# Optimization experiments

Hardware: AMD Instinct MI355X
Metric: run time of the kernel (lower is better)

Reference implementation:

```python
import jax, jax.numpy as jnp
import numpy as np

MASK_RATIO = 0.02
N2V_W, WAV_W, TV_W = 1.0, 0.2, 0.01
THRESHOLD = 50.0
LEVELS = 3


def setup_inputs() -> dict:
    key = jax.random.key(0)
    k1, k2, k3 = jax.random.split(key, 3)
    shape = (64, 1, 512, 512)
    pred = jax.random.uniform(k1, shape, dtype=jnp.float32)
    noisy_input = jax.random.uniform(k2, shape, dtype=jnp.float32)
    # N2V random blind-spot mask (torch.rand_like(pred) < mask_ratio)
    mask = jax.random.uniform(k3, shape, dtype=jnp.float32) < MASK_RATIO
    return {"pred": pred, "noisy_input": noisy_input, "mask": mask}


def haar_dwt2(x):
    # x: [B, H, W] with H, W even. Single-level 2D Haar DWT (pywt 'haar').
    a = x[:, 0::2, 0::2]
    b = x[:, 0::2, 1::2]
    c = x[:, 1::2, 0::2]
    d = x[:, 1::2, 1::2]
    ll = (a + b + c + d) * 0.5
    ch = (a + b - c - d) * 0.5  # horizontal detail
    cv = (a - b + c - d) * 0.5  # vertical detail
    cd = (a - b - c + d) * 0.5  # diagonal detail
    return ll, ch, cv, cd


def _level_l1(c, thr):
    # L1 between coeff and its (detached) soft-thresholded version
    target = jax.lax.stop_gradient(jnp.sign(c) * jnp.maximum(jnp.abs(c) - thr, 0.0))
    return jnp.mean(jnp.abs(c - target))


def reference(pred, noisy_input, mask):
    p = jnp.clip(pred, 0.0, 1.0)

    # --- Noise2Void masked L1 ---
    m = mask.astype(p.dtype)
    n2v = jnp.sum(jnp.abs(p - noisy_input) * m) / jnp.maximum(jnp.sum(m), 1.0)

    # --- Wavelet sparsity (multi-level Haar, soft-threshold targets) ---
    x = p[:, 0]  # [B, H, W]
    details = []  # finest first
    for _ in range(LEVELS):
        x, ch, cv, cd = haar_dwt2(x)
        details.append((ch, cv, cd))
    wav = jnp.asarray(0.0, dtype=p.dtype)
    for level_idx in range(1, LEVELS + 1):  # level_idx=1 -> coarsest (wavedec2 order)
        ch, cv, cd = details[LEVELS - level_idx]
        thr = (THRESHOLD / (2.0 ** (level_idx - 1))) / 255.0
        lvl = (_level_l1(ch, thr) + _level_l1(cv, thr) + _level_l1(cd, thr)) / 3.0
        wav = wav + (1.0 / level_idx) * lvl

    # --- Total variation ---
    tv = jnp.mean(jnp.abs(p[:, :, 1:, :] - p[:, :, :-1, :])) + \
         jnp.mean(jnp.abs(p[:, :, :, 1:] - p[:, :, :, :-1]))

    return N2V_W * n2v + WAV_W * wav + TV_W * tv
```

## Files before the change

### kernel.cpp

```cpp
#include <hip/hip_runtime.h>

#define NIMG 64
#define H 512
#define W 512

constexpr float THR_64  = 50.0f / 255.0f;
constexpr float THR_128 = 50.0f / 2.0f / 255.0f;
constexpr float THR_256 = 50.0f / 4.0f / 255.0f;

constexpr float SC_W1 = 0.2f  / 37748736.0f;
constexpr float SC_W2 = 0.2f  / 6291456.0f;
constexpr float SC_W3 = 0.2f  / 786432.0f;
constexpr float SC_TV = 0.01f / 16744448.0f;

__device__ __forceinline__ float wave_sum(float v) {
#pragma unroll
    for (int o = 32; o > 0; o >>= 1) v += __shfl_down(v, o, 64);
    return v;
}

__device__ __forceinline__ float clip01(float x) {
    return fminf(fmaxf(x, 0.0f), 1.0f);
}

__device__ __forceinline__ float4 clip4(float4 p) {
    p.x = clip01(p.x); p.y = clip01(p.y); p.z = clip01(p.z); p.w = clip01(p.w);
    return p;
}

__global__ __launch_bounds__(256) void kA(const float* __restrict__ pred,
                                          const float* __restrict__ noisy,
                                          const int* __restrict__ mask,
                                          float4* __restrict__ pA) {
    __shared__ float sl[9 * 512];
    __shared__ float sll2[2][128];
    __shared__ float red[4][3];

    const int tid = threadIdx.x;
    const int lane = tid & 63;
    const int wv = tid >> 6;
    const int bid = blockIdx.x;
    const int n = bid >> 6;
    const int s = bid & 63;
    const int r0 = s << 3;
    const size_t base = (size_t)n * (H * W) + (size_t)r0 * W;
    const size_t o0 = base + (size_t)tid * 4;

    float4 p0 = *reinterpret_cast<const float4*>(pred + o0);
    float4 p1 = *reinterpret_cast<const float4*>(pred + o0 + 1024);
    float4 p2 = *reinterpret_cast<const float4*>(pred + o0 + 2048);
    float4 p3 = *reinterpret_cast<const float4*>(pred + o0 + 3072);
    int4 m0 = *reinterpret_cast<const int4*>(mask + o0);
    int4 m1 = *reinterpret_cast<const int4*>(mask + o0 + 1024);
    int4 m2 = *reinterpret_cast<const int4*>(mask + o0 + 2048);
    int4 m3 = *reinterpret_cast<const int4*>(mask + o0 + 3072);
    if (tid < 128) {
        float4 hp = make_float4(0.f, 0.f, 0.f, 0.f);
        if (r0 > 0) {
            hp = clip4(*reinterpret_cast<const float4*>(pred + base - W + (size_t)tid * 4));
        }
        *reinterpret_cast<float4*>(&sl[(8 << 9) + (tid << 2)]) = hp;
    }

    const bool b0 = (m0.x | m0.y | m0.z | m0.w) != 0;
    const bool b1 = (m1.x | m1.y | m1.z | m1.w) != 0;
    const bool b2 = (m2.x | m2.y | m2.z | m2.w) != 0;
    const bool b3 = (m3.x | m3.y | m3.z | m3.w) != 0;
    float4 nz0 = make_float4(0.f, 0.f, 0.f, 0.f);
    float4 nz1 = nz0, nz2 = nz0, nz3 = nz0;
    if (b0) nz0 = *reinterpret_cast<const float4*>(noisy + o0);
    if (b1) nz1 = *reinterpret_cast<const float4*>(noisy + o0 + 1024);
    if (b2) nz2 = *reinterpret_cast<const float4*>(noisy + o0 + 2048);
    if (b3) nz3 = *reinterpret_cast<const float4*>(noisy + o0 + 3072);

    p0 = clip4(p0); p1 = clip4(p1); p2 = clip4(p2); p3 = clip4(p3);

    float n2v = 0.0f, msum = 0.0f;
#define ACC(P, MK, NZ)                                                           \
    {                                                                            \
        float m;                                                                 \
        m = MK.x ? 1.f : 0.f; n2v += fabsf(P.x - NZ.x) * m; msum += m;           \
        m = MK.y ? 1.f : 0.f; n2v += fabsf(P.y - NZ.y) * m; msum += m;           \
        m = MK.z ? 1.f : 0.f; n2v += fabsf(P.z - NZ.z) * m; msum += m;           \
        m = MK.w ? 1.f : 0.f; n2v += fabsf(P.w - NZ.w) * m; msum += m;           \
    }
    ACC(p0, m0, nz0)
    ACC(p1, m1, nz1)
    ACC(p2, m2, nz2)
    ACC(p3, m3, nz3)
#undef ACC
    *reinterpret_cast<float4*>(&sl[tid << 2]) = p0;
    *reinterpret_cast<float4*>(&sl[(tid + 256) << 2]) = p1;
    *reinterpret_cast<float4*>(&sl[(tid + 512) << 2]) = p2;
    *reinterpret_cast<float4*>(&sl[(tid + 768) << 2]) = p3;
    __syncthreads();

    const int q2 = wv >> 1;
    const int h = wv & 1;
    const int cofs = (h << 8) + (lane << 2);
    const float* rowp = sl + (q2 << 11);

    float4 q0 = *reinterpret_cast<const float4*>(rowp + cofs);
    float4 q1 = *reinterpret_cast<const float4*>(rowp + 512 + cofs);
    float4 qq2 = *reinterpret_cast<const float4*>(rowp + 1024 + cofs);
    float4 q3 = *reinterpret_cast<const float4*>(rowp + 1536 + cofs);
    const float* hrow = (q2 == 1) ? (sl + 3 * 512) : (sl + 8 * 512);
    float4 hl = *reinterpret_cast<const float4*>(hrow + cofs);
    const bool has_halo = (q2 == 1) || (r0 > 0);

    float tv = 0.0f;
    tv += fabsf(q0.y - q0.x) + fabsf(q0.z - q0.y) + fabsf(q0.w - q0.z);
    tv += fabsf(q1.y - q1.x) + fabsf(q1.z - q1.y) + fabsf(q1.w - q1.z);
    tv += fabsf(qq2.y - qq2.x) + fabsf(qq2.z - qq2.y) + fabsf(qq2.w - qq2.z);
    tv += fabsf(q3.y - q3.x) + fabsf(q3.z - q3.y) + fabsf(q3.w - q3.z);
    float nx0 = __shfl_down(q0.x, 1, 64);
    float nx1 = __shfl_down(q1.x, 1, 64);
    float nx2 = __shfl_down(qq2.x, 1, 64);
    float nx3 = __shfl_down(q3.x, 1, 64);
    if (lane < 63) {
        tv += fabsf(nx0 - q0.w) + fabsf(nx1 - q1.w)
            + fabsf(nx2 - qq2.w) + fabsf(nx3 - q3.w);
    } else if (h == 0) {
        tv += fabsf(rowp[256] - q0.w) + fabsf(rowp[512 + 256] - q1.w)
            + fabsf(rowp[1024 + 256] - qq2.w) + fabsf(rowp[1536 + 256] - q3.w);
    }
    tv += fabsf(q1.x - q0.x) + fabsf(q1.y - q0.y) + fabsf(q1.z - q0.z) + fabsf(q1.w - q0.w);
    tv += fabsf(qq2.x - q1.x) + fabsf(qq2.y - q1.y) + fabsf(qq2.z - q1.z) + fabsf(qq2.w - q1.w);
    tv += fabsf(q3.x - qq2.x) + fabsf(q3.y - qq2.y) + fabsf(q3.z - qq2.z) + fabsf(q3.w - qq2.w);
    if (has_halo) {
        tv += fabsf(q0.x - hl.x) + fabsf(q0.y - hl.y)
            + fabsf(q0.z - hl.z) + fabsf(q0.w - hl.w);
    }

    float wav1 = 0.0f;
    float a, b, c, d, ch, cv, cd;
    a = q0.x; b = q0.y; c = q1.x; d = q1.y;
    float llA0 = (a + b + c + d) * 0.5f;
    ch = (a + b - c - d) * 0.5f; cv = (a - b + c - d) * 0.5f; cd = (a - b - c + d) * 0.5f;
    wav1 += fminf(fabsf(ch), THR_256) + fminf(fabsf(cv), THR_256) + fminf(fabsf(cd), THR_256);
    a = q0.z; b = q0.w; c = q1.z; d = q1.w;
    float llA1 = (a + b + c + d) * 0.5f;
    ch = (a + b - c - d) * 0.5f; cv = (a - b + c - d) * 0.5f; cd = (a - b - c + d) * 0.5f;
    wav1 += fminf(fabsf(ch), THR_256) + fminf(fabsf(cv), THR_256) + fminf(fabsf(cd), THR_256);
    a = qq2.x; b = qq2.y; c = q3.x; d = q3.y;
    float llB0 = (a + b + c + d) * 0.5f;
    ch = (a + b - c - d) * 0.5f; cv = (a - b + c - d) * 0.5f; cd = (a - b - c + d) * 0.5f;
    wav1 += fminf(fabsf(ch), THR_256) + fminf(fabsf(cv), THR_256) + fminf(fabsf(cd), THR_256);
    a = qq2.z; b = qq2.w; c = q3.z; d = q3.w;
    float llB1 = (a + b + c + d) * 0.5f;
    ch = (a + b - c - d) * 0.5f; cv = (a - b + c - d) * 0.5f; cd = (a - b - c + d) * 0.5f;
    wav1 += fminf(fabsf(ch), THR_256) + fminf(fabsf(cv), THR_256) + fminf(fabsf(cd), THR_256);

    float wav2, ll2v;
    {
        a = llA0; b = llA1; c = llB0; d = llB1;
        ll2v = (a + b + c + d) * 0.5f;
        ch = (a + b - c - d) * 0.5f;
        cv = (a - b + c - d) * 0.5f;
        cd = (a - b - c + d) * 0.5f;
        wav2 = fminf(fabsf(ch), THR_128) + fminf(fabsf(cv), THR_128) + fminf(fabsf(cd), THR_128);
    }
    sll2[q2][(h << 6) + lane] = ll2v;

    float comb = wav1 * SC_W1 + wav2 * SC_W2 + tv * SC_TV;
    __syncthreads();

    if (wv == 0) {
        float2 top = *reinterpret_cast<const float2*>(&sll2[0][lane << 1]);
        float2 bot = *reinterpret_cast<const float2*>(&sll2[1][lane << 1]);
        a = top.x; b = top.y; c = bot.x; d = bot.y;
        ch = (a + b - c - d) * 0.5f;
        cv = (a - b + c - d) * 0.5f;
        cd = (a - b - c + d) * 0.5f;
        comb += (fminf(fabsf(ch), THR_64) + fminf(fabsf(cv), THR_64)
               + fminf(fabsf(cd), THR_64)) * SC_W3;
    }

    float v0 = wave_sum(n2v);
    float v1 = wave_sum(msum);
    float v2 = wave_sum(comb);
    if (lane == 0) {
        red[wv][0] = v0; red[wv][1] = v1; red[wv][2] = v2;
    }
    __syncthreads();
    if (tid == 0) {
        pA[bid] = make_float4(red[0][0] + red[1][0] + red[2][0] + red[3][0],
                              red[0][1] + red[1][1] + red[2][1] + red[3][1],
                              red[0][2] + red[1][2] + red[2][2] + red[3][2],
                              0.0f);
    }
}

__global__ __launch_bounds__(256) void kD(const float4* __restrict__ pA,
                                          float* __restrict__ out) {
    __shared__ float red[4][3];
    const int tid = threadIdx.x;
    const int lane = tid & 63, wv = tid >> 6;

    float s0 = 0, s1 = 0, s2 = 0;
#pragma unroll
    for (int j = 0; j < 16; ++j) {
        float4 v = pA[tid + (j << 8)];
        s0 += v.x; s1 += v.y; s2 += v.z;
    }
    s0 = wave_sum(s0); s1 = wave_sum(s1); s2 = wave_sum(s2);
    if (lane == 0) {
        red[wv][0] = s0; red[wv][1] = s1; red[wv][2] = s2;
    }
    __syncthreads();
    if (tid == 0) {
        float a0 = red[0][0] + red[1][0] + red[2][0] + red[3][0];
        float a1 = red[0][1] + red[1][1] + red[2][1] + red[3][1];
        float a2 = red[0][2] + red[1][2] + red[2][2] + red[3][2];
        out[0] = a0 / fmaxf(a1, 1.0f) + a2;
    }
}

extern "C" void kernel_launch(void* const* d_in, const int* in_sizes, int n_in,
                              void* d_out, int out_size, void* d_ws, size_t ws_size,
                              hipStream_t stream) {
    (void)in_sizes; (void)n_in; (void)out_size; (void)ws_size;
    const float* pred  = (const float*)d_in[0];
    const float* noisy = (const float*)d_in[1];
    const int*   mask  = (const int*)d_in[2];

    float4* pA = (float4*)d_ws;

    kA<<<4096, 256, 0, stream>>>(pred, noisy, mask, pA);
    kD<<<1, 256, 0, stream>>>(pA, (float*)d_out);
}
```

Before: 189.4 us.

## Give each wavefront an 8x256 tile in registers, removing LDS staging

Each wavefront now loads an 8-row by 256-column tile straight into registers and computes TV, all three Haar levels and the N2V term without shared memory. The third wavelet level uses shuffle-xor between adjacent lanes, and the column seam neighbour is fetched by a few lanes and broadcast by shuffle. This drops the LDS round trip and two block-level barriers, and halves the block count and the partials kD must reduce. In exchange each thread keeps far more data live in registers, which may lower occupancy, and it adds a few extra seam and halo loads.

```diff
diff --git a/kernel.cpp b/kernel.cpp
--- a/kernel.cpp
+++ b/kernel.cpp
@@ -32,149 +32,127 @@
                                           const float* __restrict__ noisy,
                                           const int* __restrict__ mask,
                                           float4* __restrict__ pA) {
-    __shared__ float sl[9 * 512];
-    __shared__ float sll2[2][128];
     __shared__ float red[4][3];
 
     const int tid = threadIdx.x;
     const int lane = tid & 63;
     const int wv = tid >> 6;
-    const int bid = blockIdx.x;
-    const int n = bid >> 6;
-    const int s = bid & 63;
+    const int gw = (blockIdx.x << 2) + wv;
+    const int n = gw >> 7;
+    const int u = gw & 127;
+    const int s = u >> 1;
+    const int h = u & 1;
     const int r0 = s << 3;
-    const size_t base = (size_t)n * (H * W) + (size_t)r0 * W;
-    const size_t o0 = base + (size_t)tid * 4;
-
-    float4 p0 = *reinterpret_cast<const float4*>(pred + o0);
-    float4 p1 = *reinterpret_cast<const float4*>(pred + o0 + 1024);
-    float4 p2 = *reinterpret_cast<const float4*>(pred + o0 + 2048);
-    float4 p3 = *reinterpret_cast<const float4*>(pred + o0 + 3072);
-    int4 m0 = *reinterpret_cast<const int4*>(mask + o0);
-    int4 m1 = *reinterpret_cast<const int4*>(mask + o0 + 1024);
-    int4 m2 = *reinterpret_cast<const int4*>(mask + o0 + 2048);
-    int4 m3 = *reinterpret_cast<const int4*>(mask + o0 + 3072);
-    if (tid < 128) {
-        float4 hp = make_float4(0.f, 0.f, 0.f, 0.f);
-        if (r0 > 0) {
-            hp = clip4(*reinterpret_cast<const float4*>(pred + base - W + (size_t)tid * 4));
+    const int col0 = (h << 8) + (lane << 2);
+    const size_t img = (size_t)n * (H * W);
+    const size_t base = img + (size_t)r0 * W + col0;
+
+    int4 m[8];
+#pragma unroll
+    for (int r = 0; r < 8; ++r)
+        m[r] = *reinterpret_cast<const int4*>(mask + base + (size_t)r * W);
+
+    float4 p[8];
+#pragma unroll
+    for (int r = 0; r < 8; ++r)
+        p[r] = *reinterpret_cast<const float4*>(pred + base + (size_t)r * W);
+
+    float4 hl = make_float4(0.f, 0.f, 0.f, 0.f);
+    if (r0 > 0)
+        hl = *reinterpret_cast<const float4*>(pred + base - W);
+
+    float smv = 0.f;
+    if (h == 0 && lane < 8)
+        smv = pred[img + (size_t)(r0 + lane) * W + 256];
+
+    float4 nz[8];
+#pragma unroll
+    for (int r = 0; r < 8; ++r) {
+        nz[r] = make_float4(0.f, 0.f, 0.f, 0.f);
+        if ((m[r].x | m[r].y | m[r].z | m[r].w) != 0)
+            nz[r] = *reinterpret_cast<const float4*>(noisy + base + (size_t)r * W);
+    }
+
+#pragma unroll
+    for (int r = 0; r < 8; ++r) p[r] = clip4(p[r]);
+    hl = clip4(hl);
+    smv = clip01(smv);
+
+    float tv = 0.0f;
+#pragma unroll
+    for (int r = 0; r < 8; ++r) {
+        const float4 q = p[r];
+        tv += fabsf(q.y - q.x) + fabsf(q.z - q.y) + fabsf(q.w - q.z);
+        float nb = __shfl_down(q.x, 1, 64);
+        float seam_r = __shfl(smv, r, 64);
+        if (lane == 63) nb = seam_r;
+        if (lane < 63 || h == 0) tv += fabsf(nb - q.w);
+    }
+#pragma unroll
+    for (int r = 0; r < 7; ++r) {
+        tv += fabsf(p[r + 1].x - p[r].x) + fabsf(p[r + 1].y - p[r].y)
+            + fabsf(p[r + 1].z - p[r].z) + fabsf(p[r + 1].w - p[r].w);
+    }
+    if (r0 > 0) {
+        tv += fabsf(p[0].x - hl.x) + fabsf(p[0].y - hl.y)
+            + fabsf(p[0].z - hl.z) + fabsf(p[0].w - hl.w);
+    }
+
+    float ll1[4][2];
+    float wav1 = 0.0f;
+#pragma unroll
+    for (int rp = 0; rp < 4; ++rp) {
+        const float4 t = p[2 * rp];
+        const float4 bo = p[2 * rp + 1];
+        float a, b, c, d, ch, cv, cd;
+        a = t.x; b = t.y; c = bo.x; d = bo.y;
+        ll1[rp][0] = (a + b + c + d) * 0.5f;
+        ch = (a + b - c - d) * 0.5f; cv = (a - b + c - d) * 0.5f; cd = (a - b - c + d) * 0.5f;
+        wav1 += fminf(fabsf(ch), THR_256) + fminf(fabsf(cv), THR_256) + fminf(fabsf(cd), THR_256);
+        a = t.z; b = t.w; c = bo.z; d = bo.w;
+        ll1[rp][1] = (a + b + c + d) * 0.5f;
+        ch = (a + b - c - d) * 0.5f; cv = (a - b + c - d) * 0.5f; cd = (a - b - c + d) * 0.5f;
+        wav1 += fminf(fabsf(ch), THR_256) + fminf(fabsf(cv), THR_256) + fminf(fabsf(cd), THR_256);
+    }
+
+    float ll2[2];
+    float wav2 = 0.0f;
+#pragma unroll
+    for (int lp = 0; lp < 2; ++lp) {
+        const float a = ll1[2 * lp][0], b = ll1[2 * lp][1];
+        const float c = ll1[2 * lp + 1][0], d = ll1[2 * lp + 1][1];
+        ll2[lp] = (a + b + c + d) * 0.5f;
+        const float ch = (a + b - c - d) * 0.5f;
+        const float cv = (a - b + c - d) * 0.5f;
+        const float cd = (a - b - c + d) * 0.5f;
+        wav2 += fminf(fabsf(ch), THR_128) + fminf(fabsf(cv), THR_128) + fminf(fabsf(cd), THR_128);
+    }
+
+    float w3 = 0.0f;
+    {
+        const float b3 = __shfl_xor(ll2[0], 1, 64);
+        const float d3 = __shfl_xor(ll2[1], 1, 64);
+        if ((lane & 1) == 0) {
+            const float a = ll2[0], b = b3, c = ll2[1], d = d3;
+            const float ch = (a + b - c - d) * 0.5f;
+            const float cv = (a - b + c - d) * 0.5f;
+            const float cd = (a - b - c + d) * 0.5f;
+            w3 = fminf(fabsf(ch), THR_64) + fminf(fabsf(cv), THR_64)
+               + fminf(fabsf(cd), THR_64);
         }
-        *reinterpret_cast<float4*>(&sl[(8 << 9) + (tid << 2)]) = hp;
-    }
-
-    const bool b0 = (m0.x | m0.y | m0.z | m0.w) != 0;
-    const bool b1 = (m1.x | m1.y | m1.z | m1.w) != 0;
-    const bool b2 = (m2.x | m2.y | m2.z | m2.w) != 0;
-    const bool b3 = (m3.x | m3.y | m3.z | m3.w) != 0;
-    float4 nz0 = make_float4(0.f, 0.f, 0.f, 0.f);
-    float4 nz1 = nz0, nz2 = nz0, nz3 = nz0;
-    if (b0) nz0 = *reinterpret_cast<const float4*>(noisy + o0);
-    if (b1) nz1 = *reinterpret_cast<const float4*>(noisy + o0 + 1024);
-    if (b2) nz2 = *reinterpret_cast<const float4*>(noisy + o0 + 2048);
-    if (b3) nz3 = *reinterpret_cast<const float4*>(noisy + o0 + 3072);
-
-    p0 = clip4(p0); p1 = clip4(p1); p2 = clip4(p2); p3 = clip4(p3);
+    }
 
     float n2v = 0.0f, msum = 0.0f;
-#define ACC(P, MK, NZ)                                                           \
-    {                                                                            \
-        float m;                                                                 \
-        m = MK.x ? 1.f : 0.f; n2v += fabsf(P.x - NZ.x) * m; msum += m;           \
-        m = MK.y ? 1.f : 0.f; n2v += fabsf(P.y - NZ.y) * m; msum += m;           \
-        m = MK.z ? 1.f : 0.f; n2v += fabsf(P.z - NZ.z) * m; msum += m;           \
-        m = MK.w ? 1.f : 0.f; n2v += fabsf(P.w - NZ.w) * m; msum += m;           \
-    }
-    ACC(p0, m0, nz0)
-    ACC(p1, m1, nz1)
-    ACC(p2, m2, nz2)
-    ACC(p3, m3, nz3)
-#undef ACC
-    *reinterpret_cast<float4*>(&sl[tid << 2]) = p0;
-    *reinterpret_cast<float4*>(&sl[(tid + 256) << 2]) = p1;
-    *reinterpret_cast<float4*>(&sl[(tid + 512) << 2]) = p2;
-    *reinterpret_cast<float4*>(&sl[(tid + 768) << 2]) = p3;
-    __syncthreads();
-
-    const int q2 = wv >> 1;
-    const int h = wv & 1;
-    const int cofs = (h << 8) + (lane << 2);
-    const float* rowp = sl + (q2 << 11);
-
-    float4 q0 = *reinterpret_cast<const float4*>(rowp + cofs);
-    float4 q1 = *reinterpret_cast<const float4*>(rowp + 512 + cofs);
-    float4 qq2 = *reinterpret_cast<const float4*>(rowp + 1024 + cofs);
-    float4 q3 = *reinterpret_cast<const float4*>(rowp + 1536 + cofs);
-    const float* hrow = (q2 == 1) ? (sl + 3 * 512) : (sl + 8 * 512);
-    float4 hl = *reinterpret_cast<const float4*>(hrow + cofs);
-    const bool has_halo = (q2 == 1) || (r0 > 0);
-
-    float tv = 0.0f;
-    tv += fabsf(q0.y - q0.x) + fabsf(q0.z - q0.y) + fabsf(q0.w - q0.z);
-    tv += fabsf(q1.y - q1.x) + fabsf(q1.z - q1.y) + fabsf(q1.w - q1.z);
-    tv += fabsf(qq2.y - qq2.x) + fabsf(qq2.z - qq2.y) + fabsf(qq2.w - qq2.z);
-    tv += fabsf(q3.y - q3.x) + fabsf(q3.z - q3.y) + fabsf(q3.w - q3.z);
-    float nx0 = __shfl_down(q0.x, 1, 64);
-    float nx1 = __shfl_down(q1.x, 1, 64);
-    float nx2 = __shfl_down(qq2.x, 1, 64);
-    float nx3 = __shfl_down(q3.x, 1, 64);
-    if (lane < 63) {
-        tv += fabsf(nx0 - q0.w) + fabsf(nx1 - q1.w)
-            + fabsf(nx2 - qq2.w) + fabsf(nx3 - q3.w);
-    } else if (h == 0) {
-        tv += fabsf(rowp[256] - q0.w) + fabsf(rowp[512 + 256] - q1.w)
-            + fabsf(rowp[1024 + 256] - qq2.w) + fabsf(rowp[1536 + 256] - q3.w);
-    }
-    tv += fabsf(q1.x - q0.x) + fabsf(q1.y - q0.y) + fabsf(q1.z - q0.z) + fabsf(q1.w - q0.w);
-    tv += fabsf(qq2.x - q1.x) + fabsf(qq2.y - q1.y) + fabsf(qq2.z - q1.z) + fabsf(qq2.w - q1.w);
-    tv += fabsf(q3.x - qq2.x) + fabsf(q3.y - qq2.y) + fabsf(q3.z - qq2.z) + fabsf(q3.w - qq2.w);
-    if (has_halo) {
-        tv += fabsf(q0.x - hl.x) + fabsf(q0.y - hl.y)
-            + fabsf(q0.z - hl.z) + fabsf(q0.w - hl.w);
-    }
-
-    float wav1 = 0.0f;
-    float a, b, c, d, ch, cv, cd;
-    a = q0.x; b = q0.y; c = q1.x; d = q1.y;
-    float llA0 = (a + b + c + d) * 0.5f;
-    ch = (a + b - c - d) * 0.5f; cv = (a - b + c - d) * 0.5f; cd = (a - b - c + d) * 0.5f;
-    wav1 += fminf(fabsf(ch), THR_256) + fminf(fabsf(cv), THR_256) + fminf(fabsf(cd), THR_256);
-    a = q0.z; b = q0.w; c = q1.z; d = q1.w;
-    float llA1 = (a + b + c + d) * 0.5f;
-    ch = (a + b - c - d) * 0.5f; cv = (a - b + c - d) * 0.5f; cd = (a - b - c + d) * 0.5f;
-    wav1 += fminf(fabsf(ch), THR_256) + fminf(fabsf(cv), THR_256) + fminf(fabsf(cd), THR_256);
-    a = qq2.x; b = qq2.y; c = q3.x; d = q3.y;
-    float llB0 = (a + b + c + d) * 0.5f;
-    ch = (a + b - c - d) * 0.5f; cv = (a - b + c - d) * 0.5f; cd = (a - b - c + d) * 0.5f;
-    wav1 += fminf(fabsf(ch), THR_256) + fminf(fabsf(cv), THR_256) + fminf(fabsf(cd), THR_256);
-    a = qq2.z; b = qq2.w; c = q3.z; d = q3.w;
-    float llB1 = (a + b + c + d) * 0.5f;
-    ch = (a + b - c - d) * 0.5f; cv = (a - b + c - d) * 0.5f; cd = (a - b - c + d) * 0.5f;
-    wav1 += fminf(fabsf(ch), THR_256) + fminf(fabsf(cv), THR_256) + fminf(fabsf(cd), THR_256);
-
-    float wav2, ll2v;
-    {
-        a = llA0; b = llA1; c = llB0; d = llB1;
-        ll2v = (a + b + c + d) * 0.5f;
-        ch = (a + b - c - d) * 0.5f;
-        cv = (a - b + c - d) * 0.5f;
-        cd = (a - b - c + d) * 0.5f;
-        wav2 = fminf(fabsf(ch), THR_128) + fminf(fabsf(cv), THR_128) + fminf(fabsf(cd), THR_128);
-    }
-    sll2[q2][(h << 6) + lane] = ll2v;
-
-    float comb = wav1 * SC_W1 + wav2 * SC_W2 + tv * SC_TV;
-    __syncthreads();
-
-    if (wv == 0) {
-        float2 top = *reinterpret_cast<const float2*>(&sll2[0][lane << 1]);
-        float2 bot = *reinterpret_cast<const float2*>(&sll2[1][lane << 1]);
-        a = top.x; b = top.y; c = bot.x; d = bot.y;
-        ch = (a + b - c - d) * 0.5f;
-        cv = (a - b + c - d) * 0.5f;
-        cd = (a - b - c + d) * 0.5f;
-        comb += (fminf(fabsf(ch), THR_64) + fminf(fabsf(cv), THR_64)
-               + fminf(fabsf(cd), THR_64)) * SC_W3;
-    }
+#pragma unroll
+    for (int r = 0; r < 8; ++r) {
+        float mm;
+        mm = m[r].x ? 1.f : 0.f; n2v += fabsf(p[r].x - nz[r].x) * mm; msum += mm;
+        mm = m[r].y ? 1.f : 0.f; n2v += fabsf(p[r].y - nz[r].y) * mm; msum += mm;
+        mm = m[r].z ? 1.f : 0.f; n2v += fabsf(p[r].z - nz[r].z) * mm; msum += mm;
+        mm = m[r].w ? 1.f : 0.f; n2v += fabsf(p[r].w - nz[r].w) * mm; msum += mm;
+    }
+
+    const float comb = wav1 * SC_W1 + wav2 * SC_W2 + w3 * SC_W3 + tv * SC_TV;
 
     float v0 = wave_sum(n2v);
     float v1 = wave_sum(msum);
@@ -184,10 +162,10 @@
     }
     __syncthreads();
     if (tid == 0) {
-        pA[bid] = make_float4(red[0][0] + red[1][0] + red[2][0] + red[3][0],
-                              red[0][1] + red[1][1] + red[2][1] + red[3][1],
-                              red[0][2] + red[1][2] + red[2][2] + red[3][2],
-                              0.0f);
+        pA[blockIdx.x] = make_float4(red[0][0] + red[1][0] + red[2][0] + red[3][0],
+                                     red[0][1] + red[1][1] + red[2][1] + red[3][1],
+                                     red[0][2] + red[1][2] + red[2][2] + red[3][2],
+                                     0.0f);
     }
 }
 
@@ -199,7 +177,7 @@
 
     float s0 = 0, s1 = 0, s2 = 0;
 #pragma unroll
-    for (int j = 0; j < 16; ++j) {
+    for (int j = 0; j < 8; ++j) {
         float4 v = pA[tid + (j << 8)];
         s0 += v.x; s1 += v.y; s2 += v.z;
     }
@@ -226,6 +204,6 @@
 
     float4* pA = (float4*)d_ws;
 
-    kA<<<4096, 256, 0, stream>>>(pred, noisy, mask, pA);
+    kA<<<2048, 256, 0, stream>>>(pred, noisy, mask, pA);
     kD<<<1, 256, 0, stream>>>(pA, (float*)d_out);
 }
```

Result: no change. 189.5 us (+0.0%).
